# Kernel tuning notes

Hardware: AMD Instinct MI355X
Metric: run time of the kernel (lower is better)

The kernel has to match this reference:

```python
import jax, jax.numpy as jnp
import numpy as np

N = 50000        # nodes
E = 800000       # edges
D_IN = 128       # input feature dim
HID = 64         # hidden_dim
HEADS = 4
OUT = 2          # output_dim (fraud / not-fraud)
BN_EPS = 1e-5
NEG_SLOPE = 0.2  # PyG GATv2Conv default


def setup_inputs() -> dict:
    key = jax.random.key(0)
    ks = jax.random.split(key, 16)
    g = lambda k, shape, s=0.05: (jax.random.normal(k, shape, jnp.float32) * s)
    HC = HEADS * HID  # 256
    return {
        "x": jax.random.normal(ks[0], (N, D_IN), jnp.float32),
        "edge_index": jax.random.randint(ks[1], (2, E), 0, N),
        # input projection
        "W_in": g(ks[2], (D_IN, HID)), "b_in": jnp.zeros((HID,), jnp.float32),
        # GATv2 layer 0: HID -> HID, 4 heads (concat -> 256)
        "Wl0": g(ks[3], (HID, HC)), "Wr0": g(ks[4], (HID, HC)),
        "att0": g(ks[5], (HEADS, HID)), "bias0": jnp.zeros((HC,), jnp.float32),
        # GATv2 layer 1: 256 -> HID, 4 heads (concat -> 256)
        "Wl1": g(ks[6], (HC, HC)), "Wr1": g(ks[7], (HC, HC)),
        "att1": g(ks[8], (HEADS, HID)), "bias1": jnp.zeros((HC,), jnp.float32),
        # GATv2 layer 2: 256 -> OUT, 1 head
        "Wl2": g(ks[9], (HC, OUT)), "Wr2": g(ks[10], (HC, OUT)),
        "att2": g(ks[11], (1, OUT)), "bias2": jnp.zeros((OUT,), jnp.float32),
        # BatchNorm (eval mode: running stats) for the first num_layers-1 = 2 layers
        "bn_gamma": jnp.ones((2, HC), jnp.float32),
        "bn_beta": jnp.zeros((2, HC), jnp.float32),
        "bn_mean": jnp.zeros((2, HC), jnp.float32),
        "bn_var": jnp.ones((2, HC), jnp.float32),
    }


def _gatv2(h, src, dst, Wl, Wr, att, bias):
    """PyG GATv2Conv (concat=True, negative_slope=0.2). src->dst messages."""
    n = h.shape[0]
    heads, c = att.shape
    xl = (h @ Wl).reshape(n, heads, c)   # source transform
    xr = (h @ Wr).reshape(n, heads, c)   # target transform
    e = jax.nn.leaky_relu(xl[src] + xr[dst], NEG_SLOPE)       # [E, H, C]
    logits = jnp.einsum('ehc,hc->eh', e, att)                 # [E, H]
    # segment softmax over incoming edges of each destination node
    m = jax.ops.segment_max(logits, dst, num_segments=n)      # [N, H]
    ex = jnp.exp(logits - m[dst])
    denom = jax.ops.segment_sum(ex, dst, num_segments=n)
    alpha = ex / denom[dst]                                   # [E, H]
    out = jax.ops.segment_sum(xl[src] * alpha[..., None], dst, num_segments=n)
    return out.reshape(n, heads * c) + bias


def _bn_eval(h, gamma, beta, mean, var):
    return gamma * (h - mean) * jax.lax.rsqrt(var + BN_EPS) + beta


def reference(x, edge_index, W_in, b_in, Wl0, Wr0, att0, bias0,
              Wl1, Wr1, att1, bias1, Wl2, Wr2, att2, bias2,
              bn_gamma, bn_beta, bn_mean, bn_var):
    n = x.shape[0]
    loop = jnp.arange(n)
    src = jnp.concatenate([edge_index[0], loop])  # PyG add_self_loops=True
    dst = jnp.concatenate([edge_index[1], loop])

    h = jax.nn.relu(x @ W_in + b_in)              # dropout is identity in eval

    # layer 0 (no residual: 64 != 256)
    h = _gatv2(h, src, dst, Wl0, Wr0, att0, bias0)
    h = jax.nn.relu(_bn_eval(h, bn_gamma[0], bn_beta[0], bn_mean[0], bn_var[0]))

    # layer 1 (residual: 256 == 256)
    h_prev = h
    h = _gatv2(h, src, dst, Wl1, Wr1, att1, bias1)
    h = jax.nn.relu(_bn_eval(h, bn_gamma[1], bn_beta[1], bn_mean[1], bn_var[1]))
    h = h + h_prev

    # output layer, 1 head
    h = _gatv2(h, src, dst, Wl2, Wr2, att2, bias2)
    return jax.nn.log_softmax(h, axis=1)
```

## Files before the change

kernel.cpp:

```cpp
#include <hip/hip_runtime.h>
#include <hip/hip_bf16.h>
#include <math.h>


using h16     = _Float16;
using half2v  = __attribute__((ext_vector_type(2))) h16;
using half4v  = __attribute__((ext_vector_type(4))) h16;
using half8   = __attribute__((ext_vector_type(8))) h16;
using floatx2 = __attribute__((ext_vector_type(2))) float;
using floatx4 = __attribute__((ext_vector_type(4))) float;

__device__ __forceinline__ float lrelu(float x) { return x > 0.f ? x : 0.2f * x; }

__device__ __forceinline__ half2v shfl_xor_h2(half2v v, int mask) {
    float f = __builtin_bit_cast(float, v);
    f = __shfl_xor(f, mask, 64);
    return __builtin_bit_cast(half2v, f);
}

__global__ __launch_bounds__(256) void scan_blk(const int* __restrict__ deg,
                                                int* __restrict__ rowstart,
                                                int* __restrict__ bsum, int N) {
    int t = blockIdx.x * 256 + threadIdx.x;
    int lane = threadIdx.x & 63, wid = threadIdx.x >> 6;
    int v = (t < N) ? ((deg[t] + 4) & ~3) : 0;
    int x = v;
#pragma unroll
    for (int off = 1; off < 64; off <<= 1) {
        int y = __shfl_up(x, off, 64);
        if (lane >= off) x += y;
    }
    __shared__ int wsum[4];
    if (lane == 63) wsum[wid] = x;
    __syncthreads();
    int add = 0;
#pragma unroll
    for (int w = 0; w < 4; ++w) if (w < wid) add += wsum[w];
    int incl = x + add;
    if (t < N) rowstart[t] = incl - v;
    if (threadIdx.x == 255) bsum[blockIdx.x] = incl;
}

__global__ __launch_bounds__(256) void scan_off(int* __restrict__ bsum, int NB) {
    int t = threadIdx.x;
    int lane = t & 63, wid = t >> 6;
    int v = (t < NB) ? bsum[t] : 0;
    int x = v;
#pragma unroll
    for (int off = 1; off < 64; off <<= 1) {
        int y = __shfl_up(x, off, 64);
        if (lane >= off) x += y;
    }
    __shared__ int wsum[4];
    if (lane == 63) wsum[wid] = x;
    __syncthreads();
    int add = 0;
#pragma unroll
    for (int w = 0; w < 4; ++w) if (w < wid) add += wsum[w];
    if (t < NB) bsum[t] = x + add - v;
}

__global__ void add_off(const int* __restrict__ bsum, const int* __restrict__ deg,
                        int* __restrict__ rowstart, int* __restrict__ cursor,
                        int* __restrict__ csr_src, int N) {
    int t = blockIdx.x * 256 + threadIdx.x;
    if (t >= N) return;
    int r = rowstart[t] + bsum[blockIdx.x];
    rowstart[t] = r;
    cursor[t] = r;
    int dg = deg[t];
    int npad = (dg + 4) & ~3;
    for (int k = dg; k < npad; ++k) csr_src[r + k] = t;
}

__device__ __forceinline__ void pack_one(const float* __restrict__ W,
                                         h16* __restrict__ Wp,
                                         int t, int K, int NC) {
    int j = t & 7;
    int l = (t >> 3) & 63;
    int rest = t >> 9;
    int NT = NC >> 4;
    int nt = rest % NT;
    int kc = rest / NT;
    int row = kc * 32 + (l >> 4) * 8 + j;
    int col = nt * 16 + (l & 15);
    Wp[t] = (h16)W[(size_t)row * NC + col];
}

__global__ void pack_all(const float* __restrict__ W_in,
                         const float* __restrict__ Wl0, const float* __restrict__ Wr0,
                         const float* __restrict__ Wl1, const float* __restrict__ Wr1,
                         h16* __restrict__ P_in,
                         h16* __restrict__ P_l0, h16* __restrict__ P_r0,
                         h16* __restrict__ P_l1, h16* __restrict__ P_r1,
                         const float4* __restrict__ x, half4v* __restrict__ xh, int n4,
                         const int* __restrict__ ei, int E, int* __restrict__ deg) {
    int t = blockIdx.x * blockDim.x + threadIdx.x;
    if (t < 8192)        pack_one(W_in, P_in, t, 128, 64);
    else if (t < 24576)  pack_one(Wl0, P_l0, t - 8192, 64, 256);
    else if (t < 40960)  pack_one(Wr0, P_r0, t - 24576, 64, 256);
    else if (t < 106496) pack_one(Wl1, P_l1, t - 40960, 256, 256);
    else if (t < 172032) pack_one(Wr1, P_r1, t - 106496, 256, 256);
    else if (t < 172032 + n4) {
        int u = t - 172032;
        float4 v = x[u];
        half4v o = { (h16)v.x, (h16)v.y, (h16)v.z, (h16)v.w };
        xh[u] = o;
    } else {
        int u = t - 172032 - n4;
        if (u < E) atomicAdd(&deg[ei[E + u]], 1);
    }
}

template<int KC, int NT, bool RELU>
__device__ __forceinline__ void gemm_body(const h16* __restrict__ Xh,
                                          const h16* __restrict__ Wp,
                                          const float* __restrict__ bias,
                                          h16* __restrict__ outp, int M, int bx) {
    constexpr int K = KC * 32;
    constexpr int ldo = NT * 16;
    constexpr int CHUNK8 = NT * 64;
    constexpr int PER_THR = CHUNK8 / 256;
    __shared__ half8 wbuf[2][CHUNK8];

    const half8* WG = (const half8*)Wp;
    const int tid = threadIdx.x;
    const int wid = tid >> 6, lane = tid & 63;
    const int quad = lane >> 4, li = lane & 15;
    const int r0 = bx * 64 + wid * 16;
    int arow = r0 + li; if (arow >= M) arow = M - 1;
    const half8* A8 = (const half8*)Xh + (size_t)arow * (K / 8) + quad;

    floatx4 acc[NT];
#pragma unroll
    for (int t = 0; t < NT; ++t) acc[t] = (floatx4){0.f, 0.f, 0.f, 0.f};

    half8 st[PER_THR];
#pragma unroll
    for (int i = 0; i < PER_THR; ++i) st[i] = WG[i * 256 + tid];
#pragma unroll
    for (int i = 0; i < PER_THR; ++i) wbuf[0][i * 256 + tid] = st[i];
    __syncthreads();

#pragma unroll
    for (int kc = 0; kc < KC; ++kc) {
        int cur = kc & 1;
        if (kc + 1 < KC) {
#pragma unroll
            for (int i = 0; i < PER_THR; ++i)
                st[i] = WG[(size_t)(kc + 1) * CHUNK8 + i * 256 + tid];
        }
        half8 a = A8[kc * 4];
#pragma unroll
        for (int nt = 0; nt < NT; ++nt) {
            half8 b = wbuf[cur][nt * 64 + lane];
            acc[nt] = __builtin_amdgcn_mfma_f32_16x16x32_f16(a, b, acc[nt], 0, 0, 0);
        }
        if (kc + 1 < KC) {
#pragma unroll
            for (int i = 0; i < PER_THR; ++i) wbuf[cur ^ 1][i * 256 + tid] = st[i];
        }
        __syncthreads();
    }

#pragma unroll
    for (int nt = 0; nt < NT; ++nt) {
#pragma unroll
        for (int reg = 0; reg < 4; ++reg) {
            int rr = r0 + quad * 4 + reg;
            if (rr >= M) continue;
            float v = acc[nt][reg];
            if (RELU) v = fmaxf(v + bias[nt * 16 + li], 0.f);
            outp[(size_t)rr * ldo + nt * 16 + li] = (h16)v;
        }
    }
}

template<int KC, int NT, bool RELU, bool DUAL>
__global__ __launch_bounds__(256) void gemm_lds(
        const h16* __restrict__ Xh,
        const h16* __restrict__ Wp0, const h16* __restrict__ Wp1,
        const float* __restrict__ bias,
        h16* __restrict__ out0, h16* __restrict__ out1, int M) {
    const h16* Wp = (DUAL && blockIdx.y) ? Wp1 : Wp0;
    h16* outp = (DUAL && blockIdx.y) ? out1 : out0;
    gemm_body<KC, NT, RELU>(Xh, Wp, bias, outp, M, blockIdx.x);
}

__global__ __launch_bounds__(256) void scatter_gemm0(
        const int* __restrict__ ei, int E,
        int* __restrict__ cursor, int* __restrict__ csr_src, int GS,
        const h16* __restrict__ xh, const h16* __restrict__ Wp_in,
        const float* __restrict__ b_in, h16* __restrict__ H0h, int M) {
    if ((int)blockIdx.x < GS) {
        int base = blockIdx.x * 1024 + threadIdx.x;
        int e0 = base, e1 = base + 256, e2 = base + 512, e3 = base + 768;
        int d0 = (e0 < E) ? ei[E + e0] : 0;
        int d1 = (e1 < E) ? ei[E + e1] : 0;
        int d2 = (e2 < E) ? ei[E + e2] : 0;
        int d3 = (e3 < E) ? ei[E + e3] : 0;
        int p0 = (e0 < E) ? atomicAdd(&cursor[d0], 1) : 0;
        int p1 = (e1 < E) ? atomicAdd(&cursor[d1], 1) : 0;
        int p2 = (e2 < E) ? atomicAdd(&cursor[d2], 1) : 0;
        int p3 = (e3 < E) ? atomicAdd(&cursor[d3], 1) : 0;
        int s0 = (e0 < E) ? ei[e0] : 0;
        int s1 = (e1 < E) ? ei[e1] : 0;
        int s2 = (e2 < E) ? ei[e2] : 0;
        int s3 = (e3 < E) ? ei[e3] : 0;
        if (e0 < E) csr_src[p0] = s0;
        if (e1 < E) csr_src[p1] = s1;
        if (e2 < E) csr_src[p2] = s2;
        if (e3 < E) csr_src[p3] = s3;
    } else {
        gemm_body<4, 4, true>(xh, Wp_in, b_in, H0h, M, blockIdx.x - GS);
    }
}

__global__ void attn4_bn(int N, const h16* __restrict__ XL,
                         const h16* __restrict__ XR,
                         const float* __restrict__ att,
                         const int* __restrict__ rowstart, const int* __restrict__ deg,
                         const int* __restrict__ csr_src,
                         const float* __restrict__ gamma, const float* __restrict__ beta,
                         const float* __restrict__ mean, const float* __restrict__ var,
                         const float* __restrict__ bias, const h16* __restrict__ resid,
                         h16* __restrict__ outb) {
    int wv = blockIdx.x * (blockDim.x >> 6) + (threadIdx.x >> 6);
    int d0 = wv * 2;
    if (d0 >= N) return;
    int lane = threadIdx.x & 63;
    int sl   = lane & 31;
    int dh   = d0 + (lane >> 5);
    bool dvalid = dh < N;
    int dr = dvalid ? dh : d0;

    int start = rowstart[dr];
    int dg    = deg[dr];
    int nreal = dg + 1;
    int npad  = (dg + 4) & ~3;
    int npmax = max(npad, __shfl_xor(npad, 32, 64));

    union H8 { uint4 u; half2v h[4]; };
    H8 bv, wt;
    bv.u = *(const uint4*)(XR + (size_t)dr * 256 + sl * 8);
    {
        const float* ar = att + (sl >> 3) * 64 + (sl & 7) * 8;
        float4 wa = *(const float4*)ar;
        float4 wb = *(const float4*)(ar + 4);
        wt.h[0] = half2v{(h16)wa.x, (h16)wa.y};
        wt.h[1] = half2v{(h16)wa.z, (h16)wa.w};
        wt.h[2] = half2v{(h16)wb.x, (h16)wb.y};
        wt.h[3] = half2v{(h16)wb.z, (h16)wb.w};
    }
    const h16 k02 = (h16)0.2f;
    const uint4* XLv = (const uint4*)XL;

    auto ep = [&](const H8& x) -> h16 {
        half2v q{(h16)0, (h16)0};
#pragma unroll
        for (int j = 0; j < 4; ++j) {
            half2v e  = x.h[j] + bv.h[j];
            half2v lr = __builtin_elementwise_max(e, e * k02);
            q += lr * wt.h[j];
        }
        return q.x + q.y;
    };

    float l = 0.f;
    half2v acc[4] = {half2v{(h16)0,(h16)0}, half2v{(h16)0,(h16)0},
                     half2v{(h16)0,(h16)0}, half2v{(h16)0,(h16)0}};

    int4 iv = *(const int4*)(csr_src + start);
    for (int i = 0; i < npmax; i += 4) {
        int4 cur = iv;
        if (i + 4 < npmax) {
            int nxt = min(i + 4, npad - 4);
            iv = *(const int4*)(csr_src + start + nxt);
        }
        H8 x0, x1, x2, x3;
        x0.u = XLv[(size_t)(unsigned)cur.x * 32 + sl];
        x1.u = XLv[(size_t)(unsigned)cur.y * 32 + sl];
        x2.u = XLv[(size_t)(unsigned)cur.z * 32 + sl];
        x3.u = XLv[(size_t)(unsigned)cur.w * 32 + sl];
        half2v p01 = { ep(x0), ep(x1) };
        half2v p23 = { ep(x2), ep(x3) };
#pragma unroll
        for (int s = 1; s < 8; s <<= 1) {
            p01 += shfl_xor_h2(p01, s);
            p23 += shfl_xor_h2(p23, s);
        }
        int rem = nreal - i;
        float e0 = (rem > 0) ? __expf((float)p01.x) : 0.f;
        float e1 = (rem > 1) ? __expf((float)p01.y) : 0.f;
        float e2 = (rem > 2) ? __expf((float)p23.x) : 0.f;
        float e3 = (rem > 3) ? __expf((float)p23.y) : 0.f;
        l += (e0 + e1) + (e2 + e3);
        h16 h0 = (h16)e0, h1 = (h16)e1, h2 = (h16)e2, h3 = (h16)e3;
        half2v eb0{h0,h0}, eb1{h1,h1}, eb2{h2,h2}, eb3{h3,h3};
#pragma unroll
        for (int j = 0; j < 4; ++j) {
            acc[j] += eb0 * x0.h[j];
            acc[j] += eb1 * x1.h[j];
            acc[j] += eb2 * x2.h[j];
            acc[j] += eb3 * x3.h[j];
        }
    }

    float inv = 1.f / l;
    float oc[8];
#pragma unroll
    for (int j = 0; j < 4; ++j) { oc[2*j] = (float)acc[j].x; oc[2*j+1] = (float)acc[j].y; }
    const float4* g4  = (const float4*)gamma;
    const float4* be4 = (const float4*)beta;
    const float4* mu4 = (const float4*)mean;
    const float4* va4 = (const float4*)var;
    const float4* bi4 = (const float4*)bias;
    float o[8];
#pragma unroll
    for (int q = 0; q < 2; ++q) {
        float4 g  = g4[sl*2+q],  bb = be4[sl*2+q], mu = mu4[sl*2+q];
        float4 va = va4[sl*2+q], bi = bi4[sl*2+q];
        float s0 = g.x * rsqrtf(va.x + 1e-5f);
        float s1 = g.y * rsqrtf(va.y + 1e-5f);
        float s2 = g.z * rsqrtf(va.z + 1e-5f);
        float s3 = g.w * rsqrtf(va.w + 1e-5f);
        o[q*4+0] = fmaxf(oc[q*4+0]*inv*s0 + (bi.x-mu.x)*s0 + bb.x, 0.f);
        o[q*4+1] = fmaxf(oc[q*4+1]*inv*s1 + (bi.y-mu.y)*s1 + bb.y, 0.f);
        o[q*4+2] = fmaxf(oc[q*4+2]*inv*s2 + (bi.z-mu.z)*s2 + bb.z, 0.f);
        o[q*4+3] = fmaxf(oc[q*4+3]*inv*s3 + (bi.w-mu.w)*s3 + bb.w, 0.f);
    }
    if (resid) {
        H8 rv; rv.u = *(const uint4*)(resid + (size_t)dr * 256 + sl * 8);
#pragma unroll
        for (int j = 0; j < 4; ++j) {
            o[2*j]   += (float)rv.h[j].x;
            o[2*j+1] += (float)rv.h[j].y;
        }
    }
    if (dvalid) {
        H8 ov;
#pragma unroll
        for (int j = 0; j < 4; ++j) ov.h[j] = half2v{(h16)o[2*j], (h16)o[2*j+1]};
        *(uint4*)(outb + (size_t)dh * 256 + sl * 8) = ov.u;
    }
}

__global__ void gemm2_wave(const h16* __restrict__ X, const float* __restrict__ Wl,
                           const float* __restrict__ Wr, float* __restrict__ xl2,
                           float* __restrict__ xr2, int N) {
    int t = blockIdx.x * blockDim.x + threadIdx.x;
    int n = t >> 4;
    int sl = t & 15;
    if (n >= N) return;
    const half4v* Xr = (const half4v*)(X + (size_t)n * 256);
    const float4* Wl4 = (const float4*)Wl;
    const float4* Wr4 = (const float4*)Wr;
    float l0 = 0.f, l1 = 0.f, r0 = 0.f, r1 = 0.f;
#pragma unroll
    for (int j = 0; j < 4; ++j) {
        int idx = sl + j * 16;
        half4v xh = Xr[idx];
        float4 xv = { (float)xh.x, (float)xh.y, (float)xh.z, (float)xh.w };
        float4 wa = Wl4[idx * 2];
        float4 wb = Wl4[idx * 2 + 1];
        l0 += xv.x * wa.x + xv.y * wa.z + xv.z * wb.x + xv.w * wb.z;
        l1 += xv.x * wa.y + xv.y * wa.w + xv.z * wb.y + xv.w * wb.w;
        wa = Wr4[idx * 2]; wb = Wr4[idx * 2 + 1];
        r0 += xv.x * wa.x + xv.y * wa.z + xv.z * wb.x + xv.w * wb.z;
        r1 += xv.x * wa.y + xv.y * wa.w + xv.z * wb.y + xv.w * wb.w;
    }
#pragma unroll
    for (int off = 1; off < 16; off <<= 1) {
        l0 += __shfl_xor(l0, off, 64);
        l1 += __shfl_xor(l1, off, 64);
        r0 += __shfl_xor(r0, off, 64);
        r1 += __shfl_xor(r1, off, 64);
    }
    if (sl == 0) {
        xl2[n * 2] = l0; xl2[n * 2 + 1] = l1;
        xr2[n * 2] = r0; xr2[n * 2 + 1] = r1;
    }
}

__global__ void attn1_16(int N, const float* __restrict__ xl2, const float* __restrict__ xr2,
                         const float* __restrict__ att, const float* __restrict__ bias,
                         const int* __restrict__ rowstart, const int* __restrict__ deg,
                         const int* __restrict__ csr_src, float* __restrict__ out) {
    int t = blockIdx.x * blockDim.x + threadIdx.x;
    int d = t >> 4, sl = t & 15;
    if (d >= N) return;
    float a0 = att[0], a1 = att[1];
    float2 xr = ((const float2*)xr2)[d];
    float b0 = xr.x, b1 = xr.y;
    int st = rowstart[d];
    int nreal = deg[d] + 1;
    int npad  = (deg[d] + 4) & ~3;
    float l = 0.f, ac0 = 0.f, ac1 = 0.f;
    for (int i = sl; i < npad; i += 16) {
        int s = csr_src[st + i];
        float2 xv = ((const float2*)xl2)[s];
        float q = lrelu(xv.x + b0) * a0 + lrelu(xv.y + b1) * a1;
        float e = (i < nreal) ? __expf(q) : 0.f;
        l += e; ac0 += e * xv.x; ac1 += e * xv.y;
    }
#pragma unroll
    for (int off = 1; off < 16; off <<= 1) {
        l   += __shfl_xor(l, off, 64);
        ac0 += __shfl_xor(ac0, off, 64);
        ac1 += __shfl_xor(ac1, off, 64);
    }
    if (sl == 0) {
        float inv = 1.f / l;
        float v0 = ac0 * inv + bias[0];
        float v1 = ac1 * inv + bias[1];
        float mx = fmaxf(v0, v1);
        float lse = mx + logf(__expf(v0 - mx) + __expf(v1 - mx));
        out[d * 2] = v0 - lse;
        out[d * 2 + 1] = v1 - lse;
    }
}

extern "C" void kernel_launch(void* const* d_in, const int* in_sizes, int n_in,
                              void* d_out, int out_size, void* d_ws, size_t ws_size,
                              hipStream_t stream) {
    const float* x        = (const float*)d_in[0];
    const int*   ei       = (const int*)  d_in[1];
    const float* W_in     = (const float*)d_in[2];
    const float* b_in     = (const float*)d_in[3];
    const float* Wl0      = (const float*)d_in[4];
    const float* Wr0      = (const float*)d_in[5];
    const float* att0     = (const float*)d_in[6];
    const float* bias0    = (const float*)d_in[7];
    const float* Wl1      = (const float*)d_in[8];
    const float* Wr1      = (const float*)d_in[9];
    const float* att1     = (const float*)d_in[10];
    const float* bias1    = (const float*)d_in[11];
    const float* Wl2      = (const float*)d_in[12];
    const float* Wr2      = (const float*)d_in[13];
    const float* att2     = (const float*)d_in[14];
    const float* bias2    = (const float*)d_in[15];
    const float* bn_gamma = (const float*)d_in[16];
    const float* bn_beta  = (const float*)d_in[17];
    const float* bn_mean  = (const float*)d_in[18];
    const float* bn_var   = (const float*)d_in[19];

    const int N  = in_sizes[0] / 128;
    const int E  = in_sizes[1] / 2;
    const int NB = (N + 255) / 256;

    float* ws = (float*)d_ws;
    size_t off = 0;
    float* XL2  = ws + off; off += (size_t)N * 2;
    float* XR2  = ws + off; off += (size_t)N * 2;
    h16* Ah   = (h16*)(ws + off); off += (size_t)N * 128;
    h16* Bh   = (h16*)(ws + off); off += (size_t)N * 128;
    h16* Ch   = (h16*)(ws + off); off += (size_t)N * 128;
    h16* Dh   = (h16*)(ws + off); off += (size_t)N * 128;
    h16* H0h  = (h16*)(ws + off); off += (size_t)N * 32;
    h16* xh   = (h16*)(ws + off); off += (size_t)N * 64;
    h16* Wp_in = (h16*)(ws + off); off += 4096;
    h16* Wp_l0 = (h16*)(ws + off); off += 8192;
    h16* Wp_r0 = (h16*)(ws + off); off += 8192;
    h16* Wp_l1 = (h16*)(ws + off); off += 32768;
    h16* Wp_r1 = (h16*)(ws + off); off += 32768;
    int* ip = (int*)(ws + off);
    int* deg      = ip;              ip += N;
    int* rowstart = ip;              ip += N;
    int* cursor   = ip;              ip += N;
    int* bsum     = ip;              ip += NB;
    int* csr_src  = ip;              ip += E + 4 * N + 64;

    hipMemsetAsync(deg, 0, (size_t)N * sizeof(int), stream);

    const int PACK_T = 172032 + N * 32 + E;
    pack_all<<<(PACK_T + 255) / 256, 256, 0, stream>>>(
        W_in, Wl0, Wr0, Wl1, Wr1, Wp_in, Wp_l0, Wp_r0, Wp_l1, Wp_r1,
        (const float4*)x, (half4v*)xh, N * 32, ei, E, deg);

    scan_blk<<<NB, 256, 0, stream>>>(deg, rowstart, bsum, N);
    scan_off<<<1, 256, 0, stream>>>(bsum, NB);
    add_off<<<NB, 256, 0, stream>>>(bsum, deg, rowstart, cursor, csr_src, N);

    const int GBM = (N + 63) / 64;
    const int GS  = (E + 1023) / 1024;

    scatter_gemm0<<<GS + GBM, 256, 0, stream>>>(ei, E, cursor, csr_src, GS,
                                                xh, Wp_in, b_in, H0h, N);

    gemm_lds<2, 16, false, true><<<dim3(GBM, 2), 256, 0, stream>>>(
        H0h, Wp_l0, Wp_r0, nullptr, Ah, Bh, N);
    attn4_bn<<<(N + 7) / 8, 256, 0, stream>>>(N, Ah, Bh, att0,
                                              rowstart, deg, csr_src,
                                              bn_gamma, bn_beta, bn_mean, bn_var,
                                              bias0, nullptr, Ch);

    gemm_lds<8, 16, false, true><<<dim3(GBM, 2), 256, 0, stream>>>(
        Ch, Wp_l1, Wp_r1, nullptr, Ah, Bh, N);
    attn4_bn<<<(N + 7) / 8, 256, 0, stream>>>(N, Ah, Bh, att1,
                                              rowstart, deg, csr_src,
                                              bn_gamma + 256, bn_beta + 256, bn_mean + 256,
                                              bn_var + 256, bias1, Ch, Dh);

    gemm2_wave<<<(N * 16 + 255) / 256, 256, 0, stream>>>(Dh, Wl2, Wr2, XL2, XR2, N);
    attn1_16<<<(N * 16 + 255) / 256, 256, 0, stream>>>(N, XL2, XR2, att2, bias2,
                                                       rowstart, deg, csr_src, (float*)d_out);
}
```

Measured before the change: 397.1 us.

## Widen CSR scatter per thread, shrink attention blocks, fold log2e into weights

The CSR scatter section now handles 8 edges per thread instead of 4, which halves the scatter block count and puts more atomics and loads in flight per thread. The attention kernel launches 128-thread blocks with matching launch bounds instead of 256-thread blocks, for finer scheduling granularity. The attention vector is pre-scaled by log2(e) so that exp2f can replace __expf. The pre-scaling changes fp16 rounding of the attention weights slightly, and the wider scatter raises register pressure.

```diff
diff --git a/kernel.cpp b/kernel.cpp
--- a/kernel.cpp
+++ b/kernel.cpp
@@ -193,30 +193,25 @@
         const h16* __restrict__ xh, const h16* __restrict__ Wp_in,
         const float* __restrict__ b_in, h16* __restrict__ H0h, int M) {
     if ((int)blockIdx.x < GS) {
-        int base = blockIdx.x * 1024 + threadIdx.x;
-        int e0 = base, e1 = base + 256, e2 = base + 512, e3 = base + 768;
-        int d0 = (e0 < E) ? ei[E + e0] : 0;
-        int d1 = (e1 < E) ? ei[E + e1] : 0;
-        int d2 = (e2 < E) ? ei[E + e2] : 0;
-        int d3 = (e3 < E) ? ei[E + e3] : 0;
-        int p0 = (e0 < E) ? atomicAdd(&cursor[d0], 1) : 0;
-        int p1 = (e1 < E) ? atomicAdd(&cursor[d1], 1) : 0;
-        int p2 = (e2 < E) ? atomicAdd(&cursor[d2], 1) : 0;
-        int p3 = (e3 < E) ? atomicAdd(&cursor[d3], 1) : 0;
-        int s0 = (e0 < E) ? ei[e0] : 0;
-        int s1 = (e1 < E) ? ei[e1] : 0;
-        int s2 = (e2 < E) ? ei[e2] : 0;
-        int s3 = (e3 < E) ? ei[e3] : 0;
-        if (e0 < E) csr_src[p0] = s0;
-        if (e1 < E) csr_src[p1] = s1;
-        if (e2 < E) csr_src[p2] = s2;
-        if (e3 < E) csr_src[p3] = s3;
+        int base = blockIdx.x * 2048 + threadIdx.x;
+        int e[8], d[8], p[8], s[8];
+#pragma unroll
+        for (int k = 0; k < 8; ++k) e[k] = base + k * 256;
+#pragma unroll
+        for (int k = 0; k < 8; ++k) d[k] = (e[k] < E) ? ei[E + e[k]] : 0;
+#pragma unroll
+        for (int k = 0; k < 8; ++k) p[k] = (e[k] < E) ? atomicAdd(&cursor[d[k]], 1) : 0;
+#pragma unroll
+        for (int k = 0; k < 8; ++k) s[k] = (e[k] < E) ? ei[e[k]] : 0;
+#pragma unroll
+        for (int k = 0; k < 8; ++k) if (e[k] < E) csr_src[p[k]] = s[k];
     } else {
         gemm_body<4, 4, true>(xh, Wp_in, b_in, H0h, M, blockIdx.x - GS);
     }
 }
 
-__global__ void attn4_bn(int N, const h16* __restrict__ XL,
+__global__ __launch_bounds__(128) void attn4_bn(
+                         int N, const h16* __restrict__ XL,
                          const h16* __restrict__ XR,
                          const float* __restrict__ att,
                          const int* __restrict__ rowstart, const int* __restrict__ deg,
@@ -244,13 +239,14 @@
     H8 bv, wt;
     bv.u = *(const uint4*)(XR + (size_t)dr * 256 + sl * 8);
     {
+        const float LOG2E = 1.44269504088896340736f;
         const float* ar = att + (sl >> 3) * 64 + (sl & 7) * 8;
         float4 wa = *(const float4*)ar;
         float4 wb = *(const float4*)(ar + 4);
-        wt.h[0] = half2v{(h16)wa.x, (h16)wa.y};
-        wt.h[1] = half2v{(h16)wa.z, (h16)wa.w};
-        wt.h[2] = half2v{(h16)wb.x, (h16)wb.y};
-        wt.h[3] = half2v{(h16)wb.z, (h16)wb.w};
+        wt.h[0] = half2v{(h16)(wa.x * LOG2E), (h16)(wa.y * LOG2E)};
+        wt.h[1] = half2v{(h16)(wa.z * LOG2E), (h16)(wa.w * LOG2E)};
+        wt.h[2] = half2v{(h16)(wb.x * LOG2E), (h16)(wb.y * LOG2E)};
+        wt.h[3] = half2v{(h16)(wb.z * LOG2E), (h16)(wb.w * LOG2E)};
     }
     const h16 k02 = (h16)0.2f;
     const uint4* XLv = (const uint4*)XL;
@@ -290,10 +286,10 @@
             p23 += shfl_xor_h2(p23, s);
         }
         int rem = nreal - i;
-        float e0 = (rem > 0) ? __expf((float)p01.x) : 0.f;
-        float e1 = (rem > 1) ? __expf((float)p01.y) : 0.f;
-        float e2 = (rem > 2) ? __expf((float)p23.x) : 0.f;
-        float e3 = (rem > 3) ? __expf((float)p23.y) : 0.f;
+        float e0 = (rem > 0) ? exp2f((float)p01.x) : 0.f;
+        float e1 = (rem > 1) ? exp2f((float)p01.y) : 0.f;
+        float e2 = (rem > 2) ? exp2f((float)p23.x) : 0.f;
+        float e3 = (rem > 3) ? exp2f((float)p23.y) : 0.f;
         l += (e0 + e1) + (e2 + e3);
         h16 h0 = (h16)e0, h1 = (h16)e1, h2 = (h16)e2, h3 = (h16)e3;
         half2v eb0{h0,h0}, eb1{h1,h1}, eb2{h2,h2}, eb3{h3,h3};
@@ -470,7 +466,7 @@
     int* bsum     = ip;              ip += NB;
     int* csr_src  = ip;              ip += E + 4 * N + 64;
 
-    hipMemsetAsync(deg, 0, (size_t)N * sizeof(int), stream);
+    (void)hipMemsetAsync(deg, 0, (size_t)N * sizeof(int), stream);
 
     const int PACK_T = 172032 + N * 32 + E;
     pack_all<<<(PACK_T + 255) / 256, 256, 0, stream>>>(
@@ -482,21 +478,21 @@
     add_off<<<NB, 256, 0, stream>>>(bsum, deg, rowstart, cursor, csr_src, N);
 
     const int GBM = (N + 63) / 64;
-    const int GS  = (E + 1023) / 1024;
+    const int GS  = (E + 2047) / 2048;
 
     scatter_gemm0<<<GS + GBM, 256, 0, stream>>>(ei, E, cursor, csr_src, GS,
                                                 xh, Wp_in, b_in, H0h, N);
 
     gemm_lds<2, 16, false, true><<<dim3(GBM, 2), 256, 0, stream>>>(
         H0h, Wp_l0, Wp_r0, nullptr, Ah, Bh, N);
-    attn4_bn<<<(N + 7) / 8, 256, 0, stream>>>(N, Ah, Bh, att0,
+    attn4_bn<<<(N + 3) / 4, 128, 0, stream>>>(N, Ah, Bh, att0,
                                               rowstart, deg, csr_src,
                                               bn_gamma, bn_beta, bn_mean, bn_var,
                                               bias0, nullptr, Ch);
 
     gemm_lds<8, 16, false, true><<<dim3(GBM, 2), 256, 0, stream>>>(
         Ch, Wp_l1, Wp_r1, nullptr, Ah, Bh, N);
-    attn4_bn<<<(N + 7) / 8, 256, 0, stream>>>(N, Ah, Bh, att1,
+    attn4_bn<<<(N + 3) / 4, 128, 0, stream>>>(N, Ah, Bh, att1,
                                               rowstart, deg, csr_src,
                                               bn_gamma + 256, bn_beta + 256, bn_mean + 256,
                                               bn_var + 256, bias1, Ch, Dh);
```

Result: no change. 402.8 us (+1.5%).
